# Kernel tuning notes

Measured on AMD Instinct MI355X. Metric: run time of the kernel, lower is better.

Reference implementation:

```python
import jax, jax.numpy as jnp
import numpy as np

B, S, D, N, H = 2, 1024, 1024, 16, 64
R = 2 * S          # max relative length
EPS = 1e-9
INF = 1000000.0
SHIFT = 1          # q_len == context_len branch


def _forward(query, key, value, r, cls_mask, Wq, Wk, bk, Wv, bv, Wo, bo,
             r_w_bias, r_r_bias, r_kernel, r_s_bias, seg_embed, ln_gamma, ln_beta,
             token_type_mat, attention_mask):
    scale = 1.0 / np.sqrt(H).astype(np.float32)
    q = (query @ Wq).reshape(B, S, N, H) * scale          # [b,s,n,h]
    k = (key @ Wk + bk).reshape(B, S, N, H)
    v = (value @ Wv + bv).reshape(B, S, N, H)

    # content score
    content = jnp.einsum('binh,bjnh->bnij', q + r_w_bias * scale, k)

    # relative positional score with shift-gather trick
    r_head = jnp.einsum('td,dnh->tnh', r, r_kernel)        # [2S,n,h]
    pos = jnp.einsum('binh,tnh->bnit', q + r_r_bias * scale, r_head)  # [b,n,s,2S]
    pos = pos.reshape(B, N, R, S)[:, :, SHIFT:, :].reshape(B, N, S, R - SHIFT)[..., :S]
    pos = pos * cls_mask

    # token-type (segment) score: seg_embed[0]=diff, seg_embed[1]=same
    tt_bias = jnp.einsum('binh,snh->bnis', q + r_s_bias * scale, seg_embed)  # [b,n,s,2]
    diff, same = tt_bias[..., :1], tt_bias[..., 1:]
    tt = jnp.where(token_type_mat[:, None], same, diff) * cls_mask           # [b,n,s,s]

    mask = attention_mask.astype(jnp.float32)[:, None, None]                 # [b,1,1,s]
    attn_score = content + pos + tt - INF * (1.0 - mask)
    attn_prob = jax.nn.softmax(attn_score, axis=-1)

    attn_vec = jnp.einsum('bnij,bjnh->binh', attn_prob, v).reshape(B, S, N * H)
    attn_out = attn_vec @ Wo + bo

    x = query + attn_out
    mu = jnp.mean(x, axis=-1, keepdims=True)
    var = jnp.mean(jnp.square(x - mu), axis=-1, keepdims=True)
    return (x - mu) * jax.lax.rsqrt(var + EPS) * ln_gamma + ln_beta


def setup_inputs() -> dict:
    rng = jax.random.key(0)
    ks = jax.random.split(rng, 16)
    init = 0.02
    inp = {
        'query': jax.random.normal(ks[0], (B, S, D), jnp.float32),
        'key':   jax.random.normal(ks[1], (B, S, D), jnp.float32),
        'value': jax.random.normal(ks[2], (B, S, D), jnp.float32),
        'r':     jax.random.normal(ks[3], (R, D), jnp.float32),
        'cls_mask': jnp.ones((S, S), jnp.float32),
        'Wq': jax.random.normal(ks[4], (D, N * H), jnp.float32) * init,
        'Wk': jax.random.normal(ks[5], (D, N * H), jnp.float32) * init,
        'bk': jnp.zeros((N * H,), jnp.float32),
        'Wv': jax.random.normal(ks[6], (D, N * H), jnp.float32) * init,
        'bv': jnp.zeros((N * H,), jnp.float32),
        'Wo': jax.random.normal(ks[7], (N * H, D), jnp.float32) * init,
        'bo': jnp.zeros((D,), jnp.float32),
        'r_w_bias': jax.random.normal(ks[8], (N, H), jnp.float32) * init,
        'r_r_bias': jax.random.normal(ks[9], (N, H), jnp.float32) * init,
        'r_kernel': jax.random.normal(ks[10], (D, N, H), jnp.float32) * init,
        'r_s_bias': jax.random.normal(ks[11], (N, H), jnp.float32) * init,
        'seg_embed': jax.random.normal(ks[12], (2, N, H), jnp.float32) * init,
        'ln_gamma': jnp.ones((D,), jnp.float32),
        'ln_beta': jnp.zeros((D,), jnp.float32),
        'token_type_mat': jax.random.randint(ks[13], (B, S, S), 0, 2).astype(bool),
        'attention_mask': jax.random.randint(ks[14], (B, S), 0, 2).astype(jnp.int32),
    }
    return inp


def reference(query, key, value, r, cls_mask, Wq, Wk, bk, Wv, bv, Wo, bo,
              r_w_bias, r_r_bias, r_kernel, r_s_bias, seg_embed, ln_gamma, ln_beta,
              token_type_mat, attention_mask):
    return _forward(query, key, value, r, cls_mask, Wq, Wk, bk, Wv, bv, Wo, bo,
                    r_w_bias, r_r_bias, r_kernel, r_s_bias, seg_embed, ln_gamma, ln_beta,
                    token_type_mat, attention_mask)
```

## Files before the change

### kernel.cpp

```cpp
#include <hip/hip_runtime.h>

#define S_ 1024

typedef short short8 __attribute__((ext_vector_type(8)));
typedef float floatx4 __attribute__((ext_vector_type(4)));

static __device__ __forceinline__ float b2f(ushort u) {
    union { float f; unsigned int i; } x; x.i = ((unsigned int)u) << 16; return x.f;
}
static __device__ __forceinline__ ushort f2b(float f) {
    union { float f; unsigned int i; } x; x.f = f;
    unsigned int r = (x.i + 0x7fffu + ((x.i >> 16) & 1u)) >> 16;
    return (ushort)r;
}
static __device__ __forceinline__ void async_copy16(ushort* lds, const ushort* g) {
    __builtin_amdgcn_global_load_lds((const __attribute__((address_space(1))) void*)g,
                                     (__attribute__((address_space(3))) void*)lds, 16, 0, 0);
}

struct CvtArgs { const float* src[4]; ushort* dst[4]; };
__global__ __launch_bounds__(256) void cvt_batch(CvtArgs a) {
    const float* s = a.src[blockIdx.z];
    ushort* d = a.dst[blockIdx.z];
    size_t idx = ((size_t)blockIdx.x * 256 + threadIdx.x) * 8;
    float4 f0 = *(const float4*)&s[idx];
    float4 f1 = *(const float4*)&s[idx + 4];
    alignas(16) ushort u[8] = {f2b(f0.x), f2b(f0.y), f2b(f0.z), f2b(f0.w),
                               f2b(f1.x), f2b(f1.y), f2b(f1.z), f2b(f1.w)};
    *(uint4*)&d[idx] = *(uint4*)u;
}

struct TrArgs { const float* src[4]; ushort* dst[4]; };
__global__ __launch_bounds__(256) void tr_batch(TrArgs a) {
    const float* src = a.src[blockIdx.z];
    ushort* dst = a.dst[blockIdx.z];
    __shared__ float tile[32][33];
    int bx = blockIdx.x * 32, by = blockIdx.y * 32;
    int tx = threadIdx.x & 31, ty = threadIdx.x >> 5;
#pragma unroll
    for (int i = 0; i < 32; i += 8) tile[ty + i][tx] = src[(size_t)(by + ty + i) * 1024 + bx + tx];
    __syncthreads();
#pragma unroll
    for (int i = 0; i < 32; i += 8)
        dst[(size_t)(bx + ty + i) * 1024 + by + tx] = f2b(tile[tx][ty + i]);
}

__global__ __launch_bounds__(256) void ttm_pack(const int* __restrict__ ttm,
                                                unsigned long long* __restrict__ ttb) {
    int w = threadIdx.x >> 6, lane = threadIdx.x & 63;
    int flat = blockIdx.x * 4 + w;
    unsigned long long m = __ballot(ttm[(size_t)flat * 64 + lane] != 0);
    if (lane == 0) ttb[flat] = m;
}

struct ProjArgs {
    const ushort* A[4];
    const ushort* BT[4];
    const float* bias[4];
    ushort* C[4];
    float scale[4];
};
__global__ __launch_bounds__(256, 2) void gemm_proj(ProjArgs args) {
    int z = blockIdx.z;
    const ushort* A = args.A[z];
    const ushort* BT = args.BT[z];
    const float* bias = args.bias[z];
    ushort* C = args.C[z];
    float scale = args.scale[z];

    __shared__ alignas(16) ushort As[128 * 64];
    __shared__ alignas(16) ushort Bs[128 * 64];
    int n0 = blockIdx.x * 128, m0 = blockIdx.y * 128;
    int tid = threadIdx.x, lane = tid & 63, w = tid >> 6;
    int wm = (w >> 1) * 64, wn = (w & 1) * 64;
    int li = lane & 15, q4 = lane >> 4;
    floatx4 acc[4][4] = {};
    for (int k0 = 0; k0 < 1024; k0 += 64) {
        __syncthreads();
#pragma unroll
        for (int t = 0; t < 4; t++) {
            int c = 4 * w + t;
            const ushort* ga = &A[(size_t)(m0 + 8 * c + (lane >> 3)) * 1024 + k0 + 8 * (lane & 7)];
            async_copy16(&As[c * 512 + lane * 8], ga);
            const ushort* gb = &BT[(size_t)(n0 + 8 * c + (lane >> 3)) * 1024 + k0 + 8 * (lane & 7)];
            async_copy16(&Bs[c * 512 + lane * 8], gb);
        }
        __syncthreads();
        short8 af[2][4], bf[2][4];
#pragma unroll
        for (int kk = 0; kk < 2; kk++) {
#pragma unroll
            for (int ms = 0; ms < 4; ms++)
                af[kk][ms] = *(const short8*)&As[(size_t)(wm + 16 * ms + li) * 64 + 32 * kk + 8 * q4];
#pragma unroll
            for (int ns = 0; ns < 4; ns++)
                bf[kk][ns] = *(const short8*)&Bs[(size_t)(wn + 16 * ns + li) * 64 + 32 * kk + 8 * q4];
        }
#pragma unroll
        for (int kk = 0; kk < 2; kk++)
#pragma unroll
            for (int ms = 0; ms < 4; ms++)
#pragma unroll
                for (int ns = 0; ns < 4; ns++)
                    acc[ms][ns] = __builtin_amdgcn_mfma_f32_16x16x32_bf16(af[kk][ms], bf[kk][ns],
                                                                          acc[ms][ns], 0, 0, 0);
    }
#pragma unroll
    for (int ns = 0; ns < 4; ns++) {
        int col = n0 + wn + 16 * ns + li;
        float bv = bias ? bias[col] : 0.f;
#pragma unroll
        for (int ms = 0; ms < 4; ms++)
#pragma unroll
            for (int rg = 0; rg < 4; rg++) {
                int row = m0 + wm + 16 * ms + 4 * q4 + rg;
                C[(size_t)row * 1024 + col] = f2b(acc[ms][ns][rg] * scale + bv);
            }
    }
}

__global__ __launch_bounds__(256, 2) void gemm_out(const ushort* __restrict__ A,
                                                   const ushort* __restrict__ BT,
                                                   const float* __restrict__ bias,
                                                   const float* __restrict__ resid,
                                                   float* __restrict__ X) {
    __shared__ alignas(16) ushort As[64 * 64];
    __shared__ alignas(16) ushort Bs[64 * 64];
    int n0 = blockIdx.x * 64, m0 = blockIdx.y * 64;
    int tid = threadIdx.x, lane = tid & 63, w = tid >> 6;
    int wm = (w >> 1) * 32, wn = (w & 1) * 32;
    int li = lane & 15, q4 = lane >> 4;
    floatx4 acc[2][2] = {};
    for (int k0 = 0; k0 < 1024; k0 += 64) {
        __syncthreads();
#pragma unroll
        for (int t = 0; t < 2; t++) {
            int c = 2 * w + t;
            const ushort* ga = &A[(size_t)(m0 + 8 * c + (lane >> 3)) * 1024 + k0 + 8 * (lane & 7)];
            async_copy16(&As[c * 512 + lane * 8], ga);
            const ushort* gb = &BT[(size_t)(n0 + 8 * c + (lane >> 3)) * 1024 + k0 + 8 * (lane & 7)];
            async_copy16(&Bs[c * 512 + lane * 8], gb);
        }
        __syncthreads();
        short8 af[2][2], bf[2][2];
#pragma unroll
        for (int kk = 0; kk < 2; kk++) {
#pragma unroll
            for (int ms = 0; ms < 2; ms++)
                af[kk][ms] = *(const short8*)&As[(size_t)(wm + 16 * ms + li) * 64 + 32 * kk + 8 * q4];
#pragma unroll
            for (int ns = 0; ns < 2; ns++)
                bf[kk][ns] = *(const short8*)&Bs[(size_t)(wn + 16 * ns + li) * 64 + 32 * kk + 8 * q4];
        }
#pragma unroll
        for (int kk = 0; kk < 2; kk++)
#pragma unroll
            for (int ms = 0; ms < 2; ms++)
#pragma unroll
                for (int ns = 0; ns < 2; ns++)
                    acc[ms][ns] = __builtin_amdgcn_mfma_f32_16x16x32_bf16(af[kk][ms], bf[kk][ns],
                                                                          acc[ms][ns], 0, 0, 0);
    }
#pragma unroll
    for (int ns = 0; ns < 2; ns++) {
        int col = n0 + wn + 16 * ns + li;
        float bv = bias[col];
#pragma unroll
        for (int ms = 0; ms < 2; ms++)
#pragma unroll
            for (int rg = 0; rg < 4; rg++) {
                int row = m0 + wm + 16 * ms + 4 * q4 + rg;
                X[(size_t)row * 1024 + col] = acc[ms][ns][rg] + bv + resid[(size_t)row * 1024 + col];
            }
    }
}

__global__ __launch_bounds__(256, 2) void attn_kernel(
    const ushort* __restrict__ qg, const ushort* __restrict__ kg,
    const ushort* __restrict__ vg, const ushort* __restrict__ rh,
    const float* __restrict__ rwb, const float* __restrict__ rrb,
    const float* __restrict__ rsb, const float* __restrict__ seg,
    const unsigned long long* __restrict__ ttb, const int* __restrict__ am,
    ushort* __restrict__ av) {
    __shared__ alignas(16) ushort qw[64][72];
    __shared__ alignas(16) ushort qr[64][72];
    __shared__ alignas(16) ushort kt[64][72];
    __shared__ alignas(16) ushort vt[64][72];
    __shared__ alignas(16) ushort rwin[128][72];
    __shared__ alignas(16) ushort pb[4][16][72];
    __shared__ float ttd[64], tts[64];

    int i0 = blockIdx.x * 64, n = blockIdx.y, b = blockIdx.z;
    int tid = threadIdx.x, lane = tid & 63, w = tid >> 6;
    int li = lane & 15, q4 = lane >> 4;
    const float SC = 0.125f;

    {
        int r = tid >> 2, hs = (tid & 3) * 16;
        const ushort* qp = &qg[(size_t)(b * S_ + i0 + r) * 1024 + n * 64 + hs];
        alignas(16) ushort tmp[16];
        *(uint4*)&tmp[0] = *(const uint4*)&qp[0];
        *(uint4*)&tmp[8] = *(const uint4*)&qp[8];
#pragma unroll
        for (int e = 0; e < 16; e++) {
            float qv = b2f(tmp[e]);
            qw[r][hs + e] = f2b(qv + rwb[n * 64 + hs + e] * SC);
            qr[r][hs + e] = f2b(qv + rrb[n * 64 + hs + e] * SC);
        }
    }
    __syncthreads();
    if (tid < 64) {
        float d = 0.f, s = 0.f;
        for (int h = 0; h < 64; h++) {
            float qsv = b2f(qw[tid][h]) + (rsb[n * 64 + h] - rwb[n * 64 + h]) * SC;
            d += qsv * seg[n * 64 + h];
            s += qsv * seg[1024 + n * 64 + h];
        }
        ttd[tid] = d; tts[tid] = s;
    }
    __syncthreads();

    float ttd_l[4], tts_l[4];
#pragma unroll
    for (int r = 0; r < 4; r++) { ttd_l[r] = ttd[16 * w + 4 * q4 + r]; tts_l[r] = tts[16 * w + 4 * q4 + r]; }

    floatx4 o[4] = {};
    float l_i[4] = {0.f, 0.f, 0.f, 0.f};
    const int woff = 48 - 16 * w;

    for (int j0 = 0; j0 < 1024; j0 += 64) {
        __syncthreads();
        {
            int r = tid >> 2, hs = (tid & 3) * 16;
            const ushort* kp = &kg[(size_t)(b * S_ + j0 + r) * 1024 + n * 64 + hs];
            *(uint4*)&kt[r][hs] = *(const uint4*)&kp[0];
            *(uint4*)&kt[r][hs + 8] = *(const uint4*)&kp[8];
        }
        {
            int g8 = tid >> 5, jp = tid & 31;
            const ushort* vp = &vg[(size_t)(b * S_ + j0 + 2 * jp) * 1024 + n * 64 + 8 * g8];
            uint4 va = *(const uint4*)vp;
            uint4 vb2 = *(const uint4*)(vp + 1024);
            alignas(16) ushort au[8], bu[8];
            *(uint4*)au = va; *(uint4*)bu = vb2;
#pragma unroll
            for (int e = 0; e < 8; e++) {
                unsigned int val = (unsigned int)au[e] | ((unsigned int)bu[e] << 16);
                *(unsigned int*)&vt[8 * g8 + e][2 * jp] = val;
            }
        }
        {
            int r = tid >> 1, hs = (tid & 1) * 32;
            int t = 1024 + j0 - i0 - 63 + r;
            if (t > 2047) t = 2047;
            const ushort* rp = &rh[(size_t)t * 1024 + n * 64 + hs];
            *(uint4*)&rwin[r][hs] = *(const uint4*)&rp[0];
            *(uint4*)&rwin[r][hs + 8] = *(const uint4*)&rp[8];
            *(uint4*)&rwin[r][hs + 16] = *(const uint4*)&rp[16];
            *(uint4*)&rwin[r][hs + 24] = *(const uint4*)&rp[24];
        }
        __syncthreads();

        float mb[4];
#pragma unroll
        for (int s = 0; s < 4; s++) mb[s] = am[b * S_ + j0 + 16 * s + li] ? 0.f : -1e6f;
        int wj = j0 >> 6;
        unsigned long long tb[4];
#pragma unroll
        for (int r = 0; r < 4; r++)
            tb[r] = ttb[((size_t)(b * S_) + i0 + 16 * w + 4 * q4 + r) * 16 + wj];

        short8 aw0 = *(const short8*)&qw[16 * w + li][8 * q4];
        short8 aw1 = *(const short8*)&qw[16 * w + li][32 + 8 * q4];
        floatx4 cs[4] = {};
#pragma unroll
        for (int s = 0; s < 4; s++) {
            short8 b0 = *(const short8*)&kt[16 * s + li][8 * q4];
            short8 b1 = *(const short8*)&kt[16 * s + li][32 + 8 * q4];
            cs[s] = __builtin_amdgcn_mfma_f32_16x16x32_bf16(aw0, b0, cs[s], 0, 0, 0);
            cs[s] = __builtin_amdgcn_mfma_f32_16x16x32_bf16(aw1, b1, cs[s], 0, 0, 0);
        }
        short8 ar0 = *(const short8*)&qr[16 * w + li][8 * q4];
        short8 ar1 = *(const short8*)&qr[16 * w + li][32 + 8 * q4];
        floatx4 pz[5] = {};
#pragma unroll
        for (int s5 = 0; s5 < 5; s5++) {
            short8 b0 = *(const short8*)&rwin[woff + 16 * s5 + li][8 * q4];
            short8 b1 = *(const short8*)&rwin[woff + 16 * s5 + li][32 + 8 * q4];
            pz[s5] = __builtin_amdgcn_mfma_f32_16x16x32_bf16(ar0, b0, pz[s5], 0, 0, 0);
            pz[s5] = __builtin_amdgcn_mfma_f32_16x16x32_bf16(ar1, b1, pz[s5], 0, 0, 0);
        }

        float p[4][4];
#pragma unroll
        for (int r = 0; r < 4; r++) {
            int delta = 15 - 4 * q4 - r;
            float psum = 0.f;
#pragma unroll
            for (int s = 0; s < 4; s++) {
                int c = 16 * s + li + delta;
                int srcl = (lane & 48) | (c & 15);
                float va = __shfl(pz[s][r], srcl, 64);
                float vb = __shfl(pz[s + 1][r], srcl, 64);
                float posv = ((c >> 4) == s) ? va : vb;
                float ttv = ((tb[r] >> (16 * s + li)) & 1) ? tts_l[r] : ttd_l[r];
                float sc = cs[s][r] + posv + ttv + mb[s];
                p[r][s] = __expf(sc);
                psum += p[r][s];
            }
#pragma unroll
            for (int off = 8; off >= 1; off >>= 1) psum += __shfl_xor(psum, off, 64);
            l_i[r] += psum;
        }
#pragma unroll
        for (int r = 0; r < 4; r++)
#pragma unroll
            for (int s = 0; s < 4; s++) pb[w][4 * q4 + r][16 * s + li] = f2b(p[r][s]);
#pragma unroll
        for (int ka = 0; ka < 2; ka++) {
            short8 ap = *(const short8*)&pb[w][li][32 * ka + 8 * q4];
#pragma unroll
            for (int hsub = 0; hsub < 4; hsub++) {
                short8 bv = *(const short8*)&vt[16 * hsub + li][32 * ka + 8 * q4];
                o[hsub] = __builtin_amdgcn_mfma_f32_16x16x32_bf16(ap, bv, o[hsub], 0, 0, 0);
            }
        }
    }
#pragma unroll
    for (int hsub = 0; hsub < 4; hsub++)
#pragma unroll
        for (int r = 0; r < 4; r++) {
            int i = i0 + 16 * w + 4 * q4 + r;
            int h = 16 * hsub + li;
            av[(size_t)(b * S_ + i) * 1024 + n * 64 + h] = f2b(o[hsub][r] / l_i[r]);
        }
}

__global__ __launch_bounds__(256) void ln_kernel(const float* __restrict__ X,
                                                 const float* __restrict__ gamma,
                                                 const float* __restrict__ beta,
                                                 float* __restrict__ out) {
    int row = blockIdx.x, tid = threadIdx.x;
    float4 v = *(const float4*)&X[(size_t)row * 1024 + tid * 4];
    float sum = v.x + v.y + v.z + v.w;
    float sq = v.x * v.x + v.y * v.y + v.z * v.z + v.w * v.w;
#pragma unroll
    for (int off = 32; off >= 1; off >>= 1) {
        sum += __shfl_xor(sum, off, 64);
        sq += __shfl_xor(sq, off, 64);
    }
    __shared__ float rs[4], rq[4];
    int w = tid >> 6;
    if ((tid & 63) == 0) { rs[w] = sum; rq[w] = sq; }
    __syncthreads();
    sum = rs[0] + rs[1] + rs[2] + rs[3];
    sq = rq[0] + rq[1] + rq[2] + rq[3];
    float mu = sum * (1.f / 1024.f);
    float var = sq * (1.f / 1024.f) - mu * mu;
    float rstd = rsqrtf(fmaxf(var, 0.f) + 1e-9f);
    float4 g = *(const float4*)&gamma[tid * 4];
    float4 be = *(const float4*)&beta[tid * 4];
    float4 o;
    o.x = (v.x - mu) * rstd * g.x + be.x;
    o.y = (v.y - mu) * rstd * g.y + be.y;
    o.z = (v.z - mu) * rstd * g.z + be.z;
    o.w = (v.w - mu) * rstd * g.w + be.w;
    *(float4*)&out[(size_t)row * 1024 + tid * 4] = o;
}

extern "C" void kernel_launch(void* const* d_in, const int* in_sizes, int n_in,
                              void* d_out, int out_size, void* d_ws, size_t ws_size,
                              hipStream_t stream) {
    const float* query = (const float*)d_in[0];
    const float* key   = (const float*)d_in[1];
    const float* value = (const float*)d_in[2];
    const float* r     = (const float*)d_in[3];
    const float* Wq  = (const float*)d_in[5];
    const float* Wk  = (const float*)d_in[6];
    const float* bk  = (const float*)d_in[7];
    const float* Wv  = (const float*)d_in[8];
    const float* bv  = (const float*)d_in[9];
    const float* Wo  = (const float*)d_in[10];
    const float* bo  = (const float*)d_in[11];
    const float* rwb = (const float*)d_in[12];
    const float* rrb = (const float*)d_in[13];
    const float* rk  = (const float*)d_in[14];
    const float* rsb = (const float*)d_in[15];
    const float* seg = (const float*)d_in[16];
    const float* gamma = (const float*)d_in[17];
    const float* beta  = (const float*)d_in[18];
    const int* ttm = (const int*)d_in[19];
    const int* am  = (const int*)d_in[20];
    float* out = (float*)d_out;

    char* ws = (char*)d_ws;
    const size_t MB = (size_t)1 << 20;
    ushort* WqT = (ushort*)(ws + 0 * MB);
    ushort* WkT = (ushort*)(ws + 2 * MB);
    ushort* WvT = (ushort*)(ws + 4 * MB);
    ushort* rkT = (ushort*)(ws + 6 * MB);
    ushort* qf  = (ushort*)(ws + 8 * MB);
    ushort* kf  = (ushort*)(ws + 12 * MB);
    ushort* vf  = (ushort*)(ws + 16 * MB);
    ushort* rf  = (ushort*)(ws + 20 * MB);
    ushort* qb  = (ushort*)(ws + 24 * MB);
    ushort* kb  = (ushort*)(ws + 28 * MB);
    ushort* vb  = (ushort*)(ws + 32 * MB);
    unsigned long long* ttb = (unsigned long long*)(ws + 36 * MB);
    float*  X   = (float*)(ws + 8 * MB);
    ushort* avb = (ushort*)d_out;
    ushort* rhb = (ushort*)((char*)d_out + 4 * MB);
    ushort* WoT = (ushort*)((char*)d_out + 4 * MB);

    CvtArgs ca;
    ca.src[0] = query; ca.src[1] = key; ca.src[2] = value; ca.src[3] = r;
    ca.dst[0] = qf; ca.dst[1] = kf; ca.dst[2] = vf; ca.dst[3] = rf;
    cvt_batch<<<dim3(1024, 1, 4), 256, 0, stream>>>(ca);

    TrArgs t4;
    t4.src[0] = Wq; t4.src[1] = Wk; t4.src[2] = Wv; t4.src[3] = rk;
    t4.dst[0] = WqT; t4.dst[1] = WkT; t4.dst[2] = WvT; t4.dst[3] = rkT;
    tr_batch<<<dim3(32, 32, 4), 256, 0, stream>>>(t4);

    ttm_pack<<<8192, 256, 0, stream>>>(ttm, ttb);

    ProjArgs pa;
    pa.A[0] = qf; pa.BT[0] = WqT; pa.bias[0] = nullptr; pa.C[0] = qb;  pa.scale[0] = 0.125f;
    pa.A[1] = kf; pa.BT[1] = WkT; pa.bias[1] = bk;      pa.C[1] = kb;  pa.scale[1] = 1.0f;
    pa.A[2] = vf; pa.BT[2] = WvT; pa.bias[2] = bv;      pa.C[2] = vb;  pa.scale[2] = 1.0f;
    pa.A[3] = rf; pa.BT[3] = rkT; pa.bias[3] = nullptr; pa.C[3] = rhb; pa.scale[3] = 1.0f;
    gemm_proj<<<dim3(8, 16, 4), 256, 0, stream>>>(pa);

    attn_kernel<<<dim3(16, 16, 2), 256, 0, stream>>>(qb, kb, vb, rhb, rwb, rrb, rsb, seg,
                                                     ttb, am, avb);

    TrArgs t1;
    t1.src[0] = Wo; t1.dst[0] = WoT;
    t1.src[1] = t1.src[2] = t1.src[3] = nullptr;
    t1.dst[1] = t1.dst[2] = t1.dst[3] = nullptr;
    tr_batch<<<dim3(32, 32, 1), 256, 0, stream>>>(t1);

    gemm_out<<<dim3(16, 32), 256, 0, stream>>>(avb, WoT, bo, query, X);
    ln_kernel<<<2048, 256, 0, stream>>>(X, gamma, beta, out);
}
```

Before: 252.1 us.

## Fuse preprocessing kernels, bit-pack attention mask, and cut attention LDS for occupancy

Merges the bf16 conversion, the weight transposes (now including Wo) and the token-type packing into a single pre_kernel launch. That kernel also packs the attention mask into 64-bit words. The attention kernel now keeps the q+bias operands in registers, loaded once from the reused rwin buffer, instead of the dedicated qw/qr shared arrays. It computes the segment dot products in parallel with shuffles, and it raises launch bounds to 3 blocks per SM, aiming at fewer launches and higher occupancy. The workspace layout is reshuffled so that rf lives in d_out, which adds aliasing risk.

```diff
diff --git a/kernel.cpp b/kernel.cpp
--- a/kernel.cpp
+++ b/kernel.cpp
@@ -18,39 +18,52 @@
                                      (__attribute__((address_space(3))) void*)lds, 16, 0, 0);
 }
 
-struct CvtArgs { const float* src[4]; ushort* dst[4]; };
-__global__ __launch_bounds__(256) void cvt_batch(CvtArgs a) {
-    const float* s = a.src[blockIdx.z];
-    ushort* d = a.dst[blockIdx.z];
-    size_t idx = ((size_t)blockIdx.x * 256 + threadIdx.x) * 8;
-    float4 f0 = *(const float4*)&s[idx];
-    float4 f1 = *(const float4*)&s[idx + 4];
-    alignas(16) ushort u[8] = {f2b(f0.x), f2b(f0.y), f2b(f0.z), f2b(f0.w),
-                               f2b(f1.x), f2b(f1.y), f2b(f1.z), f2b(f1.w)};
-    *(uint4*)&d[idx] = *(uint4*)u;
-}
-
-struct TrArgs { const float* src[4]; ushort* dst[4]; };
-__global__ __launch_bounds__(256) void tr_batch(TrArgs a) {
-    const float* src = a.src[blockIdx.z];
-    ushort* dst = a.dst[blockIdx.z];
-    __shared__ float tile[32][33];
-    int bx = blockIdx.x * 32, by = blockIdx.y * 32;
-    int tx = threadIdx.x & 31, ty = threadIdx.x >> 5;
-#pragma unroll
-    for (int i = 0; i < 32; i += 8) tile[ty + i][tx] = src[(size_t)(by + ty + i) * 1024 + bx + tx];
-    __syncthreads();
-#pragma unroll
-    for (int i = 0; i < 32; i += 8)
-        dst[(size_t)(bx + ty + i) * 1024 + by + tx] = f2b(tile[tx][ty + i]);
-}
-
-__global__ __launch_bounds__(256) void ttm_pack(const int* __restrict__ ttm,
-                                                unsigned long long* __restrict__ ttb) {
-    int w = threadIdx.x >> 6, lane = threadIdx.x & 63;
-    int flat = blockIdx.x * 4 + w;
-    unsigned long long m = __ballot(ttm[(size_t)flat * 64 + lane] != 0);
-    if (lane == 0) ttb[flat] = m;
+struct PreArgs {
+    const float* csrc[4]; ushort* cdst[4];
+    const float* tsrc[5]; ushort* tdst[5];
+    const int* ttm; unsigned long long* ttb;
+    const int* am;  unsigned long long* amb;
+};
+__global__ __launch_bounds__(256) void pre_kernel(PreArgs a) {
+    int z = blockIdx.z, tid = threadIdx.x;
+    if (z < 4) {
+        const float* s = a.csrc[z];
+        ushort* d = a.cdst[z];
+        size_t idx = ((size_t)blockIdx.x * 256 + tid) * 8;
+        float4 f0 = *(const float4*)&s[idx];
+        float4 f1 = *(const float4*)&s[idx + 4];
+        alignas(16) ushort u[8] = {f2b(f0.x), f2b(f0.y), f2b(f0.z), f2b(f0.w),
+                                   f2b(f1.x), f2b(f1.y), f2b(f1.z), f2b(f1.w)};
+        *(uint4*)&d[idx] = *(uint4*)u;
+    } else if (z < 9) {
+        const float* src = a.tsrc[z - 4];
+        ushort* dst = a.tdst[z - 4];
+        __shared__ float tile[32][33];
+        int bx = (blockIdx.x & 31) * 32, by = (blockIdx.x >> 5) * 32;
+        int tx = tid & 31, ty = tid >> 5;
+#pragma unroll
+        for (int i = 0; i < 32; i += 8)
+            tile[ty + i][tx] = src[(size_t)(by + ty + i) * 1024 + bx + tx];
+        __syncthreads();
+#pragma unroll
+        for (int i = 0; i < 32; i += 8)
+            dst[(size_t)(bx + ty + i) * 1024 + by + tx] = f2b(tile[tx][ty + i]);
+    } else {
+        int w = tid >> 6, lane = tid & 63;
+        int waveid = blockIdx.x * 4 + w;
+#pragma unroll
+        for (int t = 0; t < 8; t++) {
+            int word = waveid * 8 + t;
+            unsigned long long m = __ballot(a.ttm[(size_t)word * 64 + lane] != 0);
+            if (lane == 0) a.ttb[word] = m;
+        }
+        if (blockIdx.x == 0 && w == 0) {
+            for (int t = 0; t < 32; t++) {
+                unsigned long long m = __ballot(a.am[(size_t)t * 64 + lane] != 0);
+                if (lane == 0) a.amb[t] = m;
+            }
+        }
+    }
 }
 
 struct ProjArgs {
@@ -175,15 +188,13 @@
     }
 }
 
-__global__ __launch_bounds__(256, 2) void attn_kernel(
+__global__ __launch_bounds__(256, 3) void attn_kernel(
     const ushort* __restrict__ qg, const ushort* __restrict__ kg,
     const ushort* __restrict__ vg, const ushort* __restrict__ rh,
     const float* __restrict__ rwb, const float* __restrict__ rrb,
     const float* __restrict__ rsb, const float* __restrict__ seg,
-    const unsigned long long* __restrict__ ttb, const int* __restrict__ am,
+    const unsigned long long* __restrict__ ttb, const unsigned long long* __restrict__ amb,
     ushort* __restrict__ av) {
-    __shared__ alignas(16) ushort qw[64][72];
-    __shared__ alignas(16) ushort qr[64][72];
     __shared__ alignas(16) ushort kt[64][72];
     __shared__ alignas(16) ushort vt[64][72];
     __shared__ alignas(16) ushort rwin[128][72];
@@ -201,25 +212,27 @@
         alignas(16) ushort tmp[16];
         *(uint4*)&tmp[0] = *(const uint4*)&qp[0];
         *(uint4*)&tmp[8] = *(const uint4*)&qp[8];
+        float d = 0.f, s = 0.f;
 #pragma unroll
         for (int e = 0; e < 16; e++) {
             float qv = b2f(tmp[e]);
-            qw[r][hs + e] = f2b(qv + rwb[n * 64 + hs + e] * SC);
-            qr[r][hs + e] = f2b(qv + rrb[n * 64 + hs + e] * SC);
-        }
+            int h = n * 64 + hs + e;
+            rwin[r][hs + e] = f2b(qv + rwb[h] * SC);
+            rwin[64 + r][hs + e] = f2b(qv + rrb[h] * SC);
+            float qs = qv + rsb[h] * SC;
+            d += qs * seg[h];
+            s += qs * seg[1024 + h];
+        }
+        d += __shfl_xor(d, 1, 64); d += __shfl_xor(d, 2, 64);
+        s += __shfl_xor(s, 1, 64); s += __shfl_xor(s, 2, 64);
+        if ((tid & 3) == 0) { ttd[r] = d; tts[r] = s; }
     }
     __syncthreads();
-    if (tid < 64) {
-        float d = 0.f, s = 0.f;
-        for (int h = 0; h < 64; h++) {
-            float qsv = b2f(qw[tid][h]) + (rsb[n * 64 + h] - rwb[n * 64 + h]) * SC;
-            d += qsv * seg[n * 64 + h];
-            s += qsv * seg[1024 + n * 64 + h];
-        }
-        ttd[tid] = d; tts[tid] = s;
-    }
-    __syncthreads();
-
+
+    short8 aw0 = *(const short8*)&rwin[16 * w + li][8 * q4];
+    short8 aw1 = *(const short8*)&rwin[16 * w + li][32 + 8 * q4];
+    short8 ar0 = *(const short8*)&rwin[64 + 16 * w + li][8 * q4];
+    short8 ar1 = *(const short8*)&rwin[64 + 16 * w + li][32 + 8 * q4];
     float ttd_l[4], tts_l[4];
 #pragma unroll
     for (int r = 0; r < 4; r++) { ttd_l[r] = ttd[16 * w + 4 * q4 + r]; tts_l[r] = tts[16 * w + 4 * q4 + r]; }
@@ -259,19 +272,14 @@
             *(uint4*)&rwin[r][hs + 16] = *(const uint4*)&rp[16];
             *(uint4*)&rwin[r][hs + 24] = *(const uint4*)&rp[24];
         }
-        __syncthreads();
-
-        float mb[4];
-#pragma unroll
-        for (int s = 0; s < 4; s++) mb[s] = am[b * S_ + j0 + 16 * s + li] ? 0.f : -1e6f;
         int wj = j0 >> 6;
+        unsigned long long ambw = amb[b * 16 + wj];
         unsigned long long tb[4];
 #pragma unroll
         for (int r = 0; r < 4; r++)
             tb[r] = ttb[((size_t)(b * S_) + i0 + 16 * w + 4 * q4 + r) * 16 + wj];
-
-        short8 aw0 = *(const short8*)&qw[16 * w + li][8 * q4];
-        short8 aw1 = *(const short8*)&qw[16 * w + li][32 + 8 * q4];
+        __syncthreads();
+
         floatx4 cs[4] = {};
 #pragma unroll
         for (int s = 0; s < 4; s++) {
@@ -280,8 +288,6 @@
             cs[s] = __builtin_amdgcn_mfma_f32_16x16x32_bf16(aw0, b0, cs[s], 0, 0, 0);
             cs[s] = __builtin_amdgcn_mfma_f32_16x16x32_bf16(aw1, b1, cs[s], 0, 0, 0);
         }
-        short8 ar0 = *(const short8*)&qr[16 * w + li][8 * q4];
-        short8 ar1 = *(const short8*)&qr[16 * w + li][32 + 8 * q4];
         floatx4 pz[5] = {};
 #pragma unroll
         for (int s5 = 0; s5 < 5; s5++) {
@@ -304,7 +310,8 @@
                 float vb = __shfl(pz[s + 1][r], srcl, 64);
                 float posv = ((c >> 4) == s) ? va : vb;
                 float ttv = ((tb[r] >> (16 * s + li)) & 1) ? tts_l[r] : ttd_l[r];
-                float sc = cs[s][r] + posv + ttv + mb[s];
+                float mbv = ((ambw >> (16 * s + li)) & 1) ? 0.f : -1e6f;
+                float sc = cs[s][r] + posv + ttv + mbv;
                 p[r][s] = __expf(sc);
                 psum += p[r][s];
             }
@@ -399,30 +406,27 @@
     ushort* WkT = (ushort*)(ws + 2 * MB);
     ushort* WvT = (ushort*)(ws + 4 * MB);
     ushort* rkT = (ushort*)(ws + 6 * MB);
-    ushort* qf  = (ushort*)(ws + 8 * MB);
-    ushort* kf  = (ushort*)(ws + 12 * MB);
-    ushort* vf  = (ushort*)(ws + 16 * MB);
-    ushort* rf  = (ushort*)(ws + 20 * MB);
-    ushort* qb  = (ushort*)(ws + 24 * MB);
-    ushort* kb  = (ushort*)(ws + 28 * MB);
-    ushort* vb  = (ushort*)(ws + 32 * MB);
-    unsigned long long* ttb = (unsigned long long*)(ws + 36 * MB);
-    float*  X   = (float*)(ws + 8 * MB);
+    ushort* WoT = (ushort*)(ws + 8 * MB);
+    ushort* qf  = (ushort*)(ws + 10 * MB);
+    ushort* kf  = (ushort*)(ws + 14 * MB);
+    ushort* vf  = (ushort*)(ws + 18 * MB);
+    ushort* qb  = (ushort*)(ws + 22 * MB);
+    ushort* kb  = (ushort*)(ws + 26 * MB);
+    ushort* vb  = (ushort*)(ws + 30 * MB);
+    unsigned long long* ttb = (unsigned long long*)(ws + 34 * MB);
+    unsigned long long* amb = (unsigned long long*)(ws + 34 * MB + 512 * 1024);
+    float*  X   = (float*)(ws + 10 * MB);
+    ushort* rf  = (ushort*)d_out;
     ushort* avb = (ushort*)d_out;
     ushort* rhb = (ushort*)((char*)d_out + 4 * MB);
-    ushort* WoT = (ushort*)((char*)d_out + 4 * MB);
-
-    CvtArgs ca;
-    ca.src[0] = query; ca.src[1] = key; ca.src[2] = value; ca.src[3] = r;
-    ca.dst[0] = qf; ca.dst[1] = kf; ca.dst[2] = vf; ca.dst[3] = rf;
-    cvt_batch<<<dim3(1024, 1, 4), 256, 0, stream>>>(ca);
-
-    TrArgs t4;
-    t4.src[0] = Wq; t4.src[1] = Wk; t4.src[2] = Wv; t4.src[3] = rk;
-    t4.dst[0] = WqT; t4.dst[1] = WkT; t4.dst[2] = WvT; t4.dst[3] = rkT;
-    tr_batch<<<dim3(32, 32, 4), 256, 0, stream>>>(t4);
-
-    ttm_pack<<<8192, 256, 0, stream>>>(ttm, ttb);
+
+    PreArgs pr;
+    pr.csrc[0] = query; pr.csrc[1] = key; pr.csrc[2] = value; pr.csrc[3] = r;
+    pr.cdst[0] = qf; pr.cdst[1] = kf; pr.cdst[2] = vf; pr.cdst[3] = rf;
+    pr.tsrc[0] = Wq; pr.tsrc[1] = Wk; pr.tsrc[2] = Wv; pr.tsrc[3] = rk; pr.tsrc[4] = Wo;
+    pr.tdst[0] = WqT; pr.tdst[1] = WkT; pr.tdst[2] = WvT; pr.tdst[3] = rkT; pr.tdst[4] = WoT;
+    pr.ttm = ttm; pr.ttb = ttb; pr.am = am; pr.amb = amb;
+    pre_kernel<<<dim3(1024, 1, 10), 256, 0, stream>>>(pr);
 
     ProjArgs pa;
     pa.A[0] = qf; pa.BT[0] = WqT; pa.bias[0] = nullptr; pa.C[0] = qb;  pa.scale[0] = 0.125f;
@@ -432,13 +436,7 @@
     gemm_proj<<<dim3(8, 16, 4), 256, 0, stream>>>(pa);
 
     attn_kernel<<<dim3(16, 16, 2), 256, 0, stream>>>(qb, kb, vb, rhb, rwb, rrb, rsb, seg,
-                                                     ttb, am, avb);
-
-    TrArgs t1;
-    t1.src[0] = Wo; t1.dst[0] = WoT;
-    t1.src[1] = t1.src[2] = t1.src[3] = nullptr;
-    t1.dst[1] = t1.dst[2] = t1.dst[3] = nullptr;
-    tr_batch<<<dim3(32, 32, 1), 256, 0, stream>>>(t1);
+                                                     ttb, amb, avb);
 
     gemm_out<<<dim3(16, 32), 256, 0, stream>>>(avb, WoT, bo, query, X);
     ln_kernel<<<2048, 256, 0, stream>>>(X, gamma, beta, out);
```

Result: no change. 251.5 us (-0.3%).
